# Kernel optimization log

Hardware: AMD Instinct MI355X
Metric: run time of the kernel (lower is better)

The kernel has to match this reference:

```python
import jax, jax.numpy as jnp
import numpy as np
from jax import lax

NH = 8        # num_heads
NWIN = 7      # n_win
TOPK = 4


def setup_inputs() -> dict:
    key = jax.random.key(0)
    ks = jax.random.split(key, 7)
    B, C, H, W = 16, 256, 56, 56
    x = jax.random.normal(ks[0], (B, C, H, W), dtype=jnp.float32)
    s = 1.0 / np.sqrt(C)
    qkv_w = jax.random.normal(ks[1], (3 * C, C), dtype=jnp.float32) * s   # 1x1 conv
    qkv_b = jnp.zeros((3 * C,), dtype=jnp.float32)
    lepe_w = jax.random.normal(ks[2], (C, 1, 5, 5), dtype=jnp.float32) * 0.2  # depthwise 5x5
    lepe_b = jnp.zeros((C,), dtype=jnp.float32)
    out_w = jax.random.normal(ks[3], (C, C), dtype=jnp.float32) * s       # 1x1 conv
    out_b = jnp.zeros((C,), dtype=jnp.float32)
    return {"x": x, "qkv_w": qkv_w, "qkv_b": qkv_b, "lepe_w": lepe_w,
            "lepe_b": lepe_b, "out_w": out_w, "out_b": out_b}


def reference(x, qkv_w, qkv_b, lepe_w, lepe_b, out_w, out_b):
    B, C, H, W = x.shape
    rs0, rs1 = max(1, H // NWIN), max(1, W // NWIN)   # region size (H,W assumed divisible)
    rh, rw = H // rs0, W // rs1
    nreg, reg = rh * rw, rs0 * rs1
    hd = C // NH
    scale = C ** (-0.5)

    # qkv projection (1x1 conv == channel matmul)
    qkv = jnp.einsum('bchw,oc->bohw', x, qkv_w) + qkv_b[None, :, None, None]
    q, k, v = jnp.split(qkv, 3, axis=1)

    # region-level pooling (avg_pool over exact region blocks)
    def pool(t):
        return t.reshape(B, C, rh, rs0, rw, rs1).mean(axis=(3, 5))  # (B,C,rh,rw)
    q_r = pool(q).reshape(B, C, nreg).transpose(0, 2, 1)   # (B, nreg, C)
    k_r = pool(k).reshape(B, C, nreg)                      # (B, C, nreg)
    a_r = q_r @ k_r                                        # (B, nreg, nreg)
    _, idx = lax.top_k(a_r, TOPK)                          # (B, nreg, topk)

    # grid -> sequence: (B,C,H,W) -> (B,NH,nreg,reg,hd)
    def g2s(t):
        t = t.reshape(B, NH, hd, rh, rs0, rw, rs1)
        t = t.transpose(0, 1, 3, 5, 4, 6, 2)  # b,m,h,w,p,q,d
        return t.reshape(B, NH, nreg, reg, hd)

    qs, ks_, vs = g2s(q), g2s(k), g2s(v)

    # gather top-k kv regions per query region
    idx_h = jnp.broadcast_to(idx[:, None], (B, NH, nreg, TOPK))
    gidx = idx_h.reshape(B, NH, nreg * TOPK)[..., None, None]   # (B,NH,nreg*topk,1,1)
    kg = jnp.take_along_axis(ks_, gidx, axis=2).reshape(B, NH, nreg, TOPK * reg, hd)
    vg = jnp.take_along_axis(vs, gidx, axis=2).reshape(B, NH, nreg, TOPK * reg, hd)

    attn = jax.nn.softmax(jnp.einsum('bhnrd,bhnkd->bhnrk', qs * scale, kg), axis=-1)
    out = jnp.einsum('bhnrk,bhnkd->bhnrd', attn, vg)  # (B,NH,nreg,reg,hd)

    # sequence -> grid
    out = out.reshape(B, NH, rh, rw, rs0, rs1, hd)
    out = out.transpose(0, 1, 6, 2, 4, 3, 5).reshape(B, C, H, W)

    # LePE: depthwise 5x5 conv on v
    lepe = lax.conv_general_dilated(v, lepe_w, (1, 1), 'SAME',
                                    feature_group_count=C,
                                    dimension_numbers=('NCHW', 'OIHW', 'NCHW'))
    lepe = lepe + lepe_b[None, :, None, None]

    out = out + lepe
    out = jnp.einsum('bchw,oc->bohw', out, out_w) + out_b[None, :, None, None]
    return out
```

## Files before the change

kernel.cpp:

```cpp
#include <hip/hip_runtime.h>

typedef __attribute__((ext_vector_type(8))) short short8;
typedef __attribute__((ext_vector_type(4))) float f32x4;
typedef unsigned int uint;

constexpr int Bn    = 16;
constexpr int Cn    = 256;
constexpr int Hn    = 56;
constexpr int Wn    = 56;
constexpr int HWn   = Hn * Wn;
constexpr int NPn   = 3200;
constexpr int NHn   = 8;
constexpr int RWn   = 7;
constexpr int NREGn = 49;
constexpr int TOPKn = 4;
constexpr float QKSf = 0.0625f * 1.44269504088896f;

__device__ __forceinline__ float b2f(ushort u) { return __builtin_bit_cast(float, (uint)u << 16); }
__device__ __forceinline__ float b2fl(uint u) { return __builtin_bit_cast(float, u << 16); }
__device__ __forceinline__ float b2fh(uint u) { return __builtin_bit_cast(float, u & 0xffff0000u); }
__device__ __forceinline__ uint cvtpk(float lo, float hi) {
    uint r;
    asm("v_cvt_pk_bf16_f32 %0, %1, %2" : "=v"(r) : "v"(lo), "v"(hi));
    return r;
}

typedef __attribute__((address_space(3))) uint lds_u32_t;
typedef __attribute__((address_space(1))) const uint glb_u32_t;
__device__ __forceinline__ void gl_lds16(const ushort* g, ushort* l) {
    __builtin_amdgcn_global_load_lds((glb_u32_t*)g, (lds_u32_t*)l, 16, 0, 0);
}

__global__ __launch_bounds__(256)
void convert_w(const float* __restrict__ qw, const float* __restrict__ ow,
               ushort* __restrict__ wq, ushort* __restrict__ wo)
{
    const int e = (blockIdx.x * 256 + threadIdx.x) * 4;
    if (e < 196608) {
        const float4 v = *(const float4*)(qw + e);
        uint2 w; w.x = cvtpk(v.x, v.y); w.y = cvtpk(v.z, v.w);
        *(uint2*)(wq + e) = w;
    } else {
        const int e2 = e - 196608;
        const float4 v = *(const float4*)(ow + e2);
        uint2 w; w.x = cvtpk(v.x, v.y); w.y = cvtpk(v.z, v.w);
        *(uint2*)(wo + e2) = w;
    }
}

__global__ __launch_bounds__(256)
void convert_x(const float* __restrict__ x, ushort* __restrict__ xt)
{
    __shared__ float tile[64][65];
    const int p0 = blockIdx.x * 64, c0 = blockIdx.y * 64, b = blockIdx.z;
    const int tid = threadIdx.x;
    #pragma unroll
    for (int it = 0; it < 4; ++it) {
        const int slot = it * 256 + tid;
        const int c = slot >> 4, p4 = (slot & 15) << 2;
        const float4 v = *(const float4*)(x + ((size_t)b * Cn + c0 + c) * HWn + p0 + p4);
        tile[c][p4 + 0] = v.x; tile[c][p4 + 1] = v.y;
        tile[c][p4 + 2] = v.z; tile[c][p4 + 3] = v.w;
    }
    __syncthreads();
    #pragma unroll
    for (int it = 0; it < 4; ++it) {
        const int slot = it * 256 + tid;
        const int p = slot >> 4, c4 = (slot & 15) << 2;
        uint2 w;
        w.x = cvtpk(tile[c4 + 0][p], tile[c4 + 1][p]);
        w.y = cvtpk(tile[c4 + 2][p], tile[c4 + 3][p]);
        *(uint2*)(xt + ((size_t)b * NPn + p0 + p) * Cn + c0 + c4) = w;
    }
}

__global__ __launch_bounds__(256)
void pool_x(const float* __restrict__ x, float* __restrict__ xr)
{
    const int gid = blockIdx.x * 256 + threadIdx.x;
    if (gid >= Bn * Cn * NREGn) return;
    const int r = gid % NREGn;
    const int t = gid / NREGn;
    const int c = t % Cn, b = t / Cn;
    const float* plane = x + ((size_t)b * Cn + c) * HWn + (r / RWn) * 8 * Wn + (r % RWn) * 8;
    float s = 0.f;
    #pragma unroll
    for (int p = 0; p < 8; ++p) {
        const float4 a  = *(const float4*)(plane + p * Wn);
        const float4 b4 = *(const float4*)(plane + p * Wn + 4);
        s += a.x + a.y + a.z + a.w + b4.x + b4.y + b4.z + b4.w;
    }
    xr[gid] = s * (1.0f / 64.0f);
}

__global__ __launch_bounds__(256)
void qkr_gemm(const float* __restrict__ qw, const float* __restrict__ qb,
              const float* __restrict__ xr, float* __restrict__ qr,
              float* __restrict__ kr)
{
    const int gid = blockIdx.x * 256 + threadIdx.x;
    const int j = gid % NREGn;
    const int t = gid / NREGn;
    const int m = t & 511;
    const int b = t >> 9;
    const float* wr = qw + (size_t)m * Cn;
    const float* xb = xr + (size_t)b * Cn * NREGn + j;
    float s = 0.f;
    #pragma unroll 8
    for (int c = 0; c < Cn; ++c)
        s = fmaf(wr[c], xb[c * NREGn], s);
    s += qb[m];
    if (m < Cn) qr[((size_t)b * Cn + m) * NREGn + j] = s;
    else        kr[((size_t)b * Cn + (m - Cn)) * NREGn + j] = s;
}

__global__ __launch_bounds__(256)
void routing(const float* __restrict__ qr, const float* __restrict__ kr,
             int* __restrict__ idxo)
{
    const int ig = blockIdx.x, b = blockIdx.y;
    __shared__ float ksh[Cn][NREGn];
    __shared__ float qsh[Cn][7];
    __shared__ float ar[7][NREGn];
    const float* qb = qr + (size_t)b * Cn * NREGn;
    const float* kb = kr + (size_t)b * Cn * NREGn;
    for (int e = threadIdx.x; e < Cn * NREGn; e += 256)
        ksh[e / NREGn][e % NREGn] = kb[e];
    for (int e = threadIdx.x; e < Cn * 7; e += 256)
        qsh[e / 7][e % 7] = qb[(e / 7) * NREGn + ig * 7 + (e % 7)];
    __syncthreads();
    for (int e = threadIdx.x; e < 7 * NREGn; e += 256) {
        const int il = e / NREGn, j = e % NREGn;
        float s = 0.f;
        for (int c = 0; c < Cn; ++c)
            s = fmaf(qsh[c][il], ksh[c][j], s);
        ar[il][j] = s;
    }
    __syncthreads();
    if (threadIdx.x < 7) {
        const int il = threadIdx.x;
        float bv0 = -3.0e38f, bv1 = -3.0e38f, bv2 = -3.0e38f, bv3 = -3.0e38f;
        int bi0 = 0, bi1 = 0, bi2 = 0, bi3 = 0;
        for (int j = 0; j < NREGn; ++j) {
            const float v = ar[il][j];
            if (v > bv3) {
                if (v > bv0)      { bv3=bv2; bi3=bi2; bv2=bv1; bi2=bi1; bv1=bv0; bi1=bi0; bv0=v; bi0=j; }
                else if (v > bv1) { bv3=bv2; bi3=bi2; bv2=bv1; bi2=bi1; bv1=v; bi1=j; }
                else if (v > bv2) { bv3=bv2; bi3=bi2; bv2=v; bi2=j; }
                else              { bv3=v; bi3=j; }
            }
        }
        int* o = idxo + ((size_t)b * NREGn + ig * 7 + il) * TOPKn;
        o[0] = bi0; o[1] = bi1; o[2] = bi2; o[3] = bi3;
    }
}

template<int MODE>
__global__ __launch_bounds__(256)
void gemm_mfma(const ushort* __restrict__ Wb, const float* __restrict__ bias,
               const ushort* __restrict__ Bt,
               ushort* __restrict__ oq, ushort* __restrict__ ok,
               ushort* __restrict__ ovt, float* __restrict__ of)
{
    constexpr int K = Cn;
    int bb, bx, by;
    {
        const int flat = blockIdx.x;
        if (MODE == 0) {
            const int sw = (flat & 7) * 300 + (flat >> 3);
            bb = sw / 150; const int r2 = sw % 150; bx = r2 / 6; by = r2 % 6;
        } else {
            const int sw = (flat & 7) * 100 + (flat >> 3);
            bb = sw / 50;  const int r2 = sw % 50;  bx = r2 / 2; by = r2 % 2;
        }
    }
    const int n0 = bx * 128;
    const int m0 = by * 128;
    __shared__ ushort As[128 * 32];
    __shared__ ushort Bs[128 * 32];
    const int tid = threadIdx.x;
    const int wid = tid >> 6, lane = tid & 63;
    const int wm = wid >> 1, wn = wid & 1;
    const ushort* Bb = Bt + (size_t)bb * NPn * K;

    f32x4 acc[4][4];
    #pragma unroll
    for (int i = 0; i < 4; ++i)
        #pragma unroll
        for (int j = 0; j < 4; ++j)
            acc[i][j] = (f32x4){0.f, 0.f, 0.f, 0.f};

    const int cA = wid * 64 + lane;
    const int rowA = cA >> 2, koffA = (cA & 3) << 3;

    for (int k0 = 0; k0 < K; k0 += 32) {
        gl_lds16(Wb + (size_t)(m0 + rowA) * K + k0 + koffA, As + wid * 512);
        gl_lds16(Wb + (size_t)(m0 + rowA + 64) * K + k0 + koffA, As + 2048 + wid * 512);
        gl_lds16(Bb + (size_t)(n0 + rowA) * K + k0 + koffA, Bs + wid * 512);
        gl_lds16(Bb + (size_t)(n0 + rowA + 64) * K + k0 + koffA, Bs + 2048 + wid * 512);
        __syncthreads();
        short8 a[4], b[4];
        #pragma unroll
        for (int i = 0; i < 4; ++i)
            a[i] = *(const short8*)(As + (wm * 64 + i * 16 + (lane & 15)) * 32 + ((lane >> 4) << 3));
        #pragma unroll
        for (int j = 0; j < 4; ++j)
            b[j] = *(const short8*)(Bs + (wn * 64 + j * 16 + (lane & 15)) * 32 + ((lane >> 4) << 3));
        #pragma unroll
        for (int i = 0; i < 4; ++i)
            #pragma unroll
            for (int j = 0; j < 4; ++j)
                acc[i][j] = __builtin_amdgcn_mfma_f32_16x16x32_bf16(a[i], b[j], acc[i][j], 0, 0, 0);
        __syncthreads();
    }

    if (MODE == 0) {
        #pragma unroll
        for (int i = 0; i < 4; ++i) {
            const int m_base = m0 + wm * 64 + i * 16;
            const int which = m_base >> 8;
            const int hh = (m_base >> 5) & 7;
            const int db = (m_base & 31) + ((lane >> 4) << 2);
            const float4 b4 = *(const float4*)(bias + m_base + ((lane >> 4) << 2));
            #pragma unroll
            for (int j = 0; j < 4; ++j) {
                const int n = n0 + wn * 64 + j * 16 + (lane & 15);
                if (n < HWn) {
                    const int py = n / 56, px = n % 56;
                    const int rr = (py >> 3) * 7 + (px >> 3);
                    const int ss = ((py & 7) << 3) + (px & 7);
                    if (which == 0) {
                        uint2 w;
                        w.x = cvtpk((acc[i][j][0] + b4.x) * QKSf, (acc[i][j][1] + b4.y) * QKSf);
                        w.y = cvtpk((acc[i][j][2] + b4.z) * QKSf, (acc[i][j][3] + b4.w) * QKSf);
                        *(uint2*)(oq + (((size_t)bb * NHn + hh) * HWn + rr * 64 + ss) * 32 + db) = w;
                    } else if (which == 1) {
                        uint2 w;
                        w.x = cvtpk(acc[i][j][0] + b4.x, acc[i][j][1] + b4.y);
                        w.y = cvtpk(acc[i][j][2] + b4.z, acc[i][j][3] + b4.w);
                        *(uint2*)(ok + (((size_t)bb * NHn + hh) * HWn + rr * 64 + ss) * 32 + db) = w;
                    } else {
                        const size_t vtb = ((size_t)(bb * NHn + hh) * 32 + db) * HWn + rr * 64 + ss;
                        const uint lo = cvtpk(acc[i][j][0] + b4.x, acc[i][j][1] + b4.y);
                        const uint hi = cvtpk(acc[i][j][2] + b4.z, acc[i][j][3] + b4.w);
                        ovt[vtb + 0 * HWn] = (ushort)lo;
                        ovt[vtb + 1 * HWn] = (ushort)(lo >> 16);
                        ovt[vtb + 2 * HWn] = (ushort)hi;
                        ovt[vtb + 3 * HWn] = (ushort)(hi >> 16);
                    }
                }
            }
        }
    } else {
        #pragma unroll
        for (int i = 0; i < 4; ++i) {
            const int mb = m0 + wm * 64 + i * 16 + ((lane >> 4) << 2);
            const float4 b4 = *(const float4*)(bias + mb);
            #pragma unroll
            for (int j = 0; j < 4; ++j) {
                const int n = n0 + wn * 64 + j * 16 + (lane & 15);
                if (n < HWn) {
                    const int rr = n >> 6, ss = n & 63;
                    const int py = (rr / 7) * 8 + (ss >> 3);
                    const int px = (rr % 7) * 8 + (ss & 7);
                    float* od = of + ((size_t)bb * Cn + mb) * HWn + py * 56 + px;
                    od[0 * HWn] = acc[i][j][0] + b4.x;
                    od[1 * HWn] = acc[i][j][1] + b4.y;
                    od[2 * HWn] = acc[i][j][2] + b4.z;
                    od[3 * HWn] = acc[i][j][3] + b4.w;
                }
            }
        }
    }
}

__global__ __launch_bounds__(256)
void lepe(const ushort* __restrict__ vt, const float* __restrict__ lw,
          const float* __restrict__ lb, ushort* __restrict__ lbuf)
{
    const int gid = blockIdx.x * 256 + threadIdx.x;
    const int plane = gid / 392;
    const int within = gid - plane * 392;
    const int row = within / 7;
    const int sx  = within - row * 7;
    const int px0 = sx * 8;
    const int c = plane & 255;
    const ushort* vp = vt + (size_t)plane * HWn;
    const float* wc = lw + c * 25;

    float wreg[25];
    #pragma unroll
    for (int i = 0; i < 25; ++i) wreg[i] = wc[i];

    float acc[8];
    const float bias = lb[c];
    #pragma unroll
    for (int j = 0; j < 8; ++j) acc[j] = bias;

    #pragma unroll
    for (int kh = 0; kh < 5; ++kh) {
        const int iy = row + kh - 2;
        if (iy < 0 || iy >= Hn) continue;
        const int ry = iy >> 3, il = iy & 7;
        const ushort* rp = vp + (ry * 7 + sx) * 64 + il * 8;
        const uint  a = *(const uint*)(rp - 64 + 6);
        const uint4 M = *(const uint4*)(rp);
        const uint  e = *(const uint*)(rp + 64);
        float w[12];
        w[0]  = (px0 >= 2)      ? b2fl(a)   : 0.f;
        w[1]  = (px0 >= 1)      ? b2fh(a)   : 0.f;
        w[2]  = b2fl(M.x); w[3]  = b2fh(M.x);
        w[4]  = b2fl(M.y); w[5]  = b2fh(M.y);
        w[6]  = b2fl(M.z); w[7]  = b2fh(M.z);
        w[8]  = b2fl(M.w); w[9]  = b2fh(M.w);
        w[10] = (px0 + 8 < Wn)  ? b2fl(e)   : 0.f;
        w[11] = (px0 + 9 < Wn)  ? b2fh(e)   : 0.f;
        #pragma unroll
        for (int kw = 0; kw < 5; ++kw) {
            const float ww = wreg[kh * 5 + kw];
            #pragma unroll
            for (int j = 0; j < 8; ++j)
                acc[j] = fmaf(w[j + kw], ww, acc[j]);
        }
    }
    ushort* op = lbuf + (size_t)plane * HWn + ((row >> 3) * 7 + sx) * 64 + (row & 7) * 8;
    uint2 wa, wb;
    wa.x = cvtpk(acc[0], acc[1]); wa.y = cvtpk(acc[2], acc[3]);
    wb.x = cvtpk(acc[4], acc[5]); wb.y = cvtpk(acc[6], acc[7]);
    *(uint2*)(op)     = wa;
    *(uint2*)(op + 4) = wb;
}

__global__ __launch_bounds__(256, 2)
void attention3(const ushort* __restrict__ qs, const ushort* __restrict__ ks,
                const ushort* __restrict__ vt, const int* __restrict__ idxp,
                const ushort* __restrict__ lep, ushort* __restrict__ yt)
{
    const int flat = blockIdx.x;
    const int sw = (flat & 7) * 196 + (flat >> 3);
    const int b = sw / 98;
    const int rem = sw % 98;
    const int r = rem % 49;
    const int wid = threadIdx.x >> 6, lane = threadIdx.x & 63;
    const int h = (rem / 49) * 4 + wid;
    const int col = lane & 15, g = lane >> 4;
    __shared__ ushort plds_all[4][4096];
    ushort* pw = plds_all[wid];

    const size_t hb = ((size_t)b * NHn + h) * HWn;
    const size_t vtb = (size_t)(b * NHn + h) * 32;

    short8 qf[4];
    #pragma unroll
    for (int qt = 0; qt < 4; ++qt)
        qf[qt] = *(const short8*)(qs + (hb + (size_t)r * 64 + qt * 16 + col) * 32 + g * 8);

    f32x4 o[4][2];
    #pragma unroll
    for (int qt = 0; qt < 4; ++qt) {
        o[qt][0] = (f32x4){0.f, 0.f, 0.f, 0.f};
        o[qt][1] = (f32x4){0.f, 0.f, 0.f, 0.f};
    }
    float mrow[4] = {-3.0e38f, -3.0e38f, -3.0e38f, -3.0e38f};
    float lrow[4] = {0.f, 0.f, 0.f, 0.f};

    const int* ip = idxp + ((size_t)b * NREGn + r) * TOPKn;
    const int4 i4 = *(const int4*)ip;
    const int idxs[4] = {i4.x, i4.y, i4.z, i4.w};

    short8 kfA[4], vfA[4];
    {
        const int rr = idxs[0];
        #pragma unroll
        for (int kt = 0; kt < 4; ++kt)
            kfA[kt] = *(const short8*)(ks + (hb + (size_t)rr * 64 + kt * 16 + col) * 32 + g * 8);
        #pragma unroll
        for (int dt = 0; dt < 2; ++dt)
            #pragma unroll
            for (int kc = 0; kc < 2; ++kc)
                vfA[dt * 2 + kc] = *(const short8*)(vt + (vtb + dt * 16 + col) * HWn
                                                    + (size_t)rr * 64 + kc * 32 + g * 8);
    }

    #pragma unroll
    for (int t = 0; t < TOPKn; ++t) {
        short8 kfB[4], vfB[4];
        if (t < 3) {
            const int rr = idxs[t + 1];
            #pragma unroll
            for (int kt = 0; kt < 4; ++kt)
                kfB[kt] = *(const short8*)(ks + (hb + (size_t)rr * 64 + kt * 16 + col) * 32 + g * 8);
            #pragma unroll
            for (int dt = 0; dt < 2; ++dt)
                #pragma unroll
                for (int kc = 0; kc < 2; ++kc)
                    vfB[dt * 2 + kc] = *(const short8*)(vt + (vtb + dt * 16 + col) * HWn
                                                         + (size_t)rr * 64 + kc * 32 + g * 8);
        }

        #pragma unroll
        for (int qt = 0; qt < 4; ++qt) {
            f32x4 s[4];
            #pragma unroll
            for (int kt = 0; kt < 4; ++kt)
                s[kt] = __builtin_amdgcn_mfma_f32_16x16x32_bf16(
                    kfA[kt], qf[qt], (f32x4){0.f, 0.f, 0.f, 0.f}, 0, 0, 0);

            float mx = s[0][0];
            #pragma unroll
            for (int kt = 0; kt < 4; ++kt)
                #pragma unroll
                for (int e = 0; e < 4; ++e)
                    mx = fmaxf(mx, s[kt][e]);
            mx = fmaxf(mx, __shfl_xor(mx, 16));
            mx = fmaxf(mx, __shfl_xor(mx, 32));
            if (!__all(mx - mrow[qt] <= 8.f)) {
                const float mnew = fmaxf(mrow[qt], mx);
                const float corr = exp2f(mrow[qt] - mnew);
                mrow[qt] = mnew;
                lrow[qt] *= corr;
                #pragma unroll
                for (int reg = 0; reg < 4; ++reg) {
                    const float cr = __shfl(corr, g * 4 + reg);
                    o[qt][0][reg] *= cr;
                    o[qt][1][reg] *= cr;
                }
            }
            float ps = 0.f;
            #pragma unroll
            for (int kt = 0; kt < 4; ++kt)
                #pragma unroll
                for (int e = 0; e < 4; ++e) {
                    const float p = exp2f(s[kt][e] - mrow[qt]);
                    s[kt][e] = p; ps += p;
                }
            ps += __shfl_xor(ps, 16);
            ps += __shfl_xor(ps, 32);
            lrow[qt] += ps;
            const int qrow = qt * 16 + col;
            const int swz = (qrow & 7) << 4;
            #pragma unroll
            for (int kt = 0; kt < 4; ++kt) {
                uint2 pk;
                pk.x = cvtpk(s[kt][0], s[kt][1]);
                pk.y = cvtpk(s[kt][2], s[kt][3]);
                const int byt = (qrow * 128 + kt * 32 + g * 8) ^ swz;
                *(uint2*)((char*)pw + byt) = pk;
            }
        }

        #pragma unroll
        for (int kc = 0; kc < 2; ++kc)
            #pragma unroll
            for (int qt = 0; qt < 4; ++qt) {
                const int qrow = qt * 16 + col;
                const int byt = (qrow * 128 + kc * 64 + g * 16) ^ ((qrow & 7) << 4);
                const short8 pf = *(const short8*)((const char*)pw + byt);
                o[qt][0] = __builtin_amdgcn_mfma_f32_16x16x32_bf16(pf, vfA[0 * 2 + kc], o[qt][0], 0, 0, 0);
                o[qt][1] = __builtin_amdgcn_mfma_f32_16x16x32_bf16(pf, vfA[1 * 2 + kc], o[qt][1], 0, 0, 0);
            }

        if (t < 3) {
            #pragma unroll
            for (int i = 0; i < 4; ++i) { kfA[i] = kfB[i]; vfA[i] = vfB[i]; }
        }
    }

    #pragma unroll
    for (int qt = 0; qt < 4; ++qt) {
        const float linv = 1.0f / lrow[qt];
        #pragma unroll
        for (int reg = 0; reg < 4; ++reg) {
            const float li = __shfl(linv, g * 4 + reg);
            const int row = qt * 16 + g * 4 + reg;
            const int swz = ((row >> 1) & 3) << 4;
            const uint pk = cvtpk(o[qt][0][reg] * li, o[qt][1][reg] * li);
            const int byt0 = (row * 64 + col * 2) ^ swz;
            const int byt1 = (row * 64 + (16 + col) * 2) ^ swz;
            *(ushort*)((char*)pw + byt0) = (ushort)pk;
            *(ushort*)((char*)pw + byt1) = (ushort)(pk >> 16);
        }
    }
    const ushort* lp = lep + ((size_t)b * Cn + h * 32) * HWn + (size_t)r * 64 + lane;
    ushort* yp = yt + ((size_t)b * NPn + (size_t)r * 64 + lane) * Cn + h * 32;
    const int swl = ((lane >> 1) & 3) << 4;
    #pragma unroll
    for (int c4 = 0; c4 < 8; ++c4) {
        const int byt = (lane * 64 + c4 * 8) ^ swl;
        const ushort4 ov = *(const ushort4*)((const char*)pw + byt);
        const float a0 = b2f(ov.x) + b2f(lp[(size_t)(c4 * 4 + 0) * HWn]);
        const float a1 = b2f(ov.y) + b2f(lp[(size_t)(c4 * 4 + 1) * HWn]);
        const float a2 = b2f(ov.z) + b2f(lp[(size_t)(c4 * 4 + 2) * HWn]);
        const float a3 = b2f(ov.w) + b2f(lp[(size_t)(c4 * 4 + 3) * HWn]);
        uint2 w4; w4.x = cvtpk(a0, a1); w4.y = cvtpk(a2, a3);
        *(uint2*)(yp + c4 * 4) = w4;
    }
}

extern "C" void kernel_launch(void* const* d_in, const int* in_sizes, int n_in,
                              void* d_out, int out_size, void* d_ws, size_t ws_size,
                              hipStream_t stream)
{
    const float* x      = (const float*)d_in[0];
    const float* qkv_w  = (const float*)d_in[1];
    const float* qkv_b  = (const float*)d_in[2];
    const float* lepe_w = (const float*)d_in[3];
    const float* lepe_b = (const float*)d_in[4];
    const float* out_w  = (const float*)d_in[5];
    const float* out_b  = (const float*)d_in[6];
    float* out = (float*)d_out;

    char* ws = (char*)d_ws;
    ushort* XT = (ushort*)(ws);
    ushort* YT = (ushort*)(ws + 26214400);
    ushort* QS = (ushort*)(ws + 52428800);
    ushort* KS = (ushort*)(ws + 78118912);
    ushort* VT = (ushort*)(ws + 103809024);
    ushort* LB = (ushort*)(ws + 129499136);
    ushort* WQ = (ushort*)(ws + 155189248);
    ushort* WO = (ushort*)(ws + 155582464);
    float*  XR = (float*)(ws + 155713536);
    float*  QR = (float*)(ws + 156516352);
    float*  KR = (float*)(ws + 157319168);
    int*   IDX = (int*)(ws + 158121984);

    convert_w<<<256, 256, 0, stream>>>(qkv_w, out_w, WQ, WO);
    convert_x<<<dim3(49, 4, 16), 256, 0, stream>>>(x, XT);
    pool_x<<<(Bn * Cn * NREGn + 255) / 256, 256, 0, stream>>>(x, XR);
    qkr_gemm<<<1568, 256, 0, stream>>>(qkv_w, qkv_b, XR, QR, KR);
    routing<<<dim3(7, 16), 256, 0, stream>>>(QR, KR, IDX);
    gemm_mfma<0><<<2400, 256, 0, stream>>>(WQ, qkv_b, XT, QS, KS, VT, nullptr);
    lepe<<<6272, 256, 0, stream>>>(VT, lepe_w, lepe_b, LB);
    attention3<<<1568, 256, 0, stream>>>(QS, KS, VT, IDX, LB, YT);
    gemm_mfma<1><<<800, 256, 0, stream>>>(WO, out_b, YT, nullptr, nullptr, nullptr, out);
}
```

Baseline: 243.5 us.

## Fuse region pooling partials into convert_x and double-buffer GEMM LDS tiles

convert_x now also produces per-row 8-pixel partial sums from its shared tile, and a small reduce_pool kernel assembles the region means from those partials. This replaces the old pool_x kernel, which re-read the whole fp32 input from global memory. Separately, gemm_mfma double-buffers its A and B LDS tiles so the next k-slice's global-to-LDS loads are issued before the current slice's MFMAs. The cost is extra workspace for the partials, double the GEMM shared memory (which may lower occupancy), and more complex index logic in reduce_pool.

Measured after the change: 243.9 us. About the same (+0.2%).

```diff
diff --git a/kernel.cpp b/kernel.cpp
--- a/kernel.cpp
+++ b/kernel.cpp
@@ -49,7 +49,8 @@
 }
 
 __global__ __launch_bounds__(256)
-void convert_x(const float* __restrict__ x, ushort* __restrict__ xt)
+void convert_x(const float* __restrict__ x, ushort* __restrict__ xt,
+               float* __restrict__ part)
 {
     __shared__ float tile[64][65];
     const int p0 = blockIdx.x * 64, c0 = blockIdx.y * 64, b = blockIdx.z;
@@ -72,23 +73,33 @@
         w.y = cvtpk(tile[c4 + 2][p], tile[c4 + 3][p]);
         *(uint2*)(xt + ((size_t)b * NPn + p0 + p) * Cn + c0 + c4) = w;
     }
-}
-
-__global__ __launch_bounds__(256)
-void pool_x(const float* __restrict__ x, float* __restrict__ xr)
+    {
+        const int c = tid >> 2, q = tid & 3;
+        float sA = 0.f, sB = 0.f;
+        #pragma unroll
+        for (int p = 0; p < 8; ++p) sA += tile[c][q * 16 + p];
+        #pragma unroll
+        for (int p = 0; p < 8; ++p) sB += tile[c][q * 16 + 8 + p];
+        float* pp = part + ((((size_t)b * 4 + blockIdx.y) * 49 + blockIdx.x) * 64 + c) * 8 + q * 2;
+        *(float2*)pp = make_float2(sA, sB);
+    }
+}
+
+__global__ __launch_bounds__(256)
+void reduce_pool(const float* __restrict__ part, float* __restrict__ xr)
 {
     const int gid = blockIdx.x * 256 + threadIdx.x;
-    if (gid >= Bn * Cn * NREGn) return;
     const int r = gid % NREGn;
     const int t = gid / NREGn;
     const int c = t % Cn, b = t / Cn;
-    const float* plane = x + ((size_t)b * Cn + c) * HWn + (r / RWn) * 8 * Wn + (r % RWn) * 8;
+    const int ry = r / 7, rx = r % 7;
+    const float* pb = part + ((((size_t)b * 4 + (c >> 6)) * 49 + 7 * ry) * 64 + (c & 63)) * 8;
     float s = 0.f;
     #pragma unroll
-    for (int p = 0; p < 8; ++p) {
-        const float4 a  = *(const float4*)(plane + p * Wn);
-        const float4 b4 = *(const float4*)(plane + p * Wn + 4);
-        s += a.x + a.y + a.z + a.w + b4.x + b4.y + b4.z + b4.w;
+    for (int j = 0; j < 7; ++j) {
+        const int s0 = (rx - j + 7) % 7;
+        s += pb[j * 512 + s0];
+        if (s0 == 0) s += pb[j * 512 + 7];
     }
     xr[gid] = s * (1.0f / 64.0f);
 }
@@ -176,8 +187,8 @@
     }
     const int n0 = bx * 128;
     const int m0 = by * 128;
-    __shared__ ushort As[128 * 32];
-    __shared__ ushort Bs[128 * 32];
+    __shared__ ushort As[2][4096];
+    __shared__ ushort Bs[2][4096];
     const int tid = threadIdx.x;
     const int wid = tid >> 6, lane = tid & 63;
     const int wm = wid >> 1, wn = wid & 1;
@@ -193,19 +204,31 @@
     const int cA = wid * 64 + lane;
     const int rowA = cA >> 2, koffA = (cA & 3) << 3;
 
-    for (int k0 = 0; k0 < K; k0 += 32) {
-        gl_lds16(Wb + (size_t)(m0 + rowA) * K + k0 + koffA, As + wid * 512);
-        gl_lds16(Wb + (size_t)(m0 + rowA + 64) * K + k0 + koffA, As + 2048 + wid * 512);
-        gl_lds16(Bb + (size_t)(n0 + rowA) * K + k0 + koffA, Bs + wid * 512);
-        gl_lds16(Bb + (size_t)(n0 + rowA + 64) * K + k0 + koffA, Bs + 2048 + wid * 512);
-        __syncthreads();
+    const ushort* wA0 = Wb + (size_t)(m0 + rowA) * K + koffA;
+    const ushort* wA1 = Wb + (size_t)(m0 + rowA + 64) * K + koffA;
+    const ushort* bB0 = Bb + (size_t)(n0 + rowA) * K + koffA;
+    const ushort* bB1 = Bb + (size_t)(n0 + rowA + 64) * K + koffA;
+
+#define STAGE(buf, k0)                                              \
+    do {                                                            \
+        gl_lds16(wA0 + (k0), &As[buf][wid * 512]);                  \
+        gl_lds16(wA1 + (k0), &As[buf][2048 + wid * 512]);           \
+        gl_lds16(bB0 + (k0), &Bs[buf][wid * 512]);                  \
+        gl_lds16(bB1 + (k0), &Bs[buf][2048 + wid * 512]);           \
+    } while (0)
+
+    STAGE(0, 0);
+    __syncthreads();
+    int cur = 0;
+    for (int k0 = 0; k0 < K; k0 += 32, cur ^= 1) {
+        if (k0 + 32 < K) STAGE(cur ^ 1, k0 + 32);
         short8 a[4], b[4];
         #pragma unroll
         for (int i = 0; i < 4; ++i)
-            a[i] = *(const short8*)(As + (wm * 64 + i * 16 + (lane & 15)) * 32 + ((lane >> 4) << 3));
+            a[i] = *(const short8*)(&As[cur][(wm * 64 + i * 16 + (lane & 15)) * 32 + ((lane >> 4) << 3)]);
         #pragma unroll
         for (int j = 0; j < 4; ++j)
-            b[j] = *(const short8*)(Bs + (wn * 64 + j * 16 + (lane & 15)) * 32 + ((lane >> 4) << 3));
+            b[j] = *(const short8*)(&Bs[cur][(wn * 64 + j * 16 + (lane & 15)) * 32 + ((lane >> 4) << 3)]);
         #pragma unroll
         for (int i = 0; i < 4; ++i)
             #pragma unroll
@@ -213,6 +236,7 @@
                 acc[i][j] = __builtin_amdgcn_mfma_f32_16x16x32_bf16(a[i], b[j], acc[i][j], 0, 0, 0);
         __syncthreads();
     }
+#undef STAGE
 
     if (MODE == 0) {
         #pragma unroll
@@ -523,10 +547,11 @@
     float*  QR = (float*)(ws + 156516352);
     float*  KR = (float*)(ws + 157319168);
     int*   IDX = (int*)(ws + 158121984);
+    float* PART = (float*)(ws + 158134528);
 
     convert_w<<<256, 256, 0, stream>>>(qkv_w, out_w, WQ, WO);
-    convert_x<<<dim3(49, 4, 16), 256, 0, stream>>>(x, XT);
-    pool_x<<<(Bn * Cn * NREGn + 255) / 256, 256, 0, stream>>>(x, XR);
+    convert_x<<<dim3(49, 4, 16), 256, 0, stream>>>(x, XT, PART);
+    reduce_pool<<<784, 256, 0, stream>>>(PART, XR);
     qkr_gemm<<<1568, 256, 0, stream>>>(qkv_w, qkv_b, XR, QR, KR);
     routing<<<dim3(7, 16), 256, 0, stream>>>(QR, KR, IDX);
     gemm_mfma<0><<<2400, 256, 0, stream>>>(WQ, qkv_b, XT, QS, KS, VT, nullptr);
```
